# Performance work log

Measured on AMD Instinct MI355X. Metric: run time of the kernel, lower is better.

Reference implementation:

```python
import jax, jax.numpy as jnp
import numpy as np

CLS_W, REG_W, OBJ_W = 1.0, 5.0, 1.0
NUM_CLASSES = 30
B, N = 16, 64
SCALES = [(80, 80), (40, 40), (20, 20)]


def setup_inputs() -> dict:
    key = jax.random.key(0)
    ks = jax.random.split(key, 12)
    inp = {}
    for i, (h, w) in enumerate(SCALES):
        inp[f"cls_p{i}"] = jax.random.normal(ks[3 * i + 0], (B, NUM_CLASSES, h, w), jnp.float32)
        inp[f"reg_p{i}"] = jax.random.normal(ks[3 * i + 1], (B, 4, h, w), jnp.float32)
        inp[f"obj_p{i}"] = jax.random.normal(ks[3 * i + 2], (B, 1, h, w), jnp.float32)
    inp["boxes"] = jax.random.uniform(ks[9], (B, N, 4), jnp.float32)  # normalized cxcywh in [0,1)
    inp["labels"] = jax.random.randint(ks[10], (B, N), 0, NUM_CLASSES, jnp.int32)
    return inp


def _scale_losses(cls_p, reg_p, obj_p, boxes, labels):
    Bs, C, H, W = cls_p.shape
    # BCHW -> flat (B*H*W, C) to mirror the permute(0,2,3,1)
    cls_f = jnp.transpose(cls_p, (0, 2, 3, 1)).reshape(-1, C)
    reg_f = jnp.transpose(reg_p, (0, 2, 3, 1)).reshape(-1, 4)
    obj_f = jnp.transpose(obj_p, (0, 2, 3, 1)).reshape(-1)
    # grid assignment: int() truncation == floor for non-negative coords, then clamp
    gx = jnp.clip((boxes[..., 0] * W).astype(jnp.int32), 0, W - 1)
    gy = jnp.clip((boxes[..., 1] * H).astype(jnp.int32), 0, H - 1)
    bidx = jnp.arange(Bs, dtype=jnp.int32)[:, None]
    flat = ((bidx * H + gy) * W + gx).reshape(-1)  # [B*N] flat cell ids
    M = Bs * H * W
    obj_t = jnp.zeros((M,), cls_p.dtype).at[flat].set(1.0)
    reg_t = jnp.zeros((M, 4), cls_p.dtype).at[flat].set(boxes.reshape(-1, 4))
    cls_t = jnp.zeros((M, C), cls_p.dtype).at[flat, labels.reshape(-1)].set(1.0)
    pos = obj_t > 0.5
    npos = jnp.maximum(pos.sum().astype(cls_p.dtype), 1.0)
    # cross-entropy on positive cells (argmax of one-hot target, ties -> lowest idx as in torch)
    cls_idx = jnp.argmax(cls_t, axis=-1)
    ce = jax.nn.logsumexp(cls_f, axis=-1) - jnp.take_along_axis(cls_f, cls_idx[:, None], axis=-1)[:, 0]
    cls_loss = jnp.sum(jnp.where(pos, ce, 0.0)) / npos * CLS_W
    # smooth-L1 (beta=1), mean over 4 coords, clamp at 10, mean over positives
    d = jnp.abs(reg_f - reg_t)
    sl1 = jnp.mean(jnp.where(d < 1.0, 0.5 * d * d, d - 0.5), axis=-1)
    sl1 = jnp.minimum(sl1, 10.0)
    reg_loss = jnp.sum(jnp.where(pos, sl1, 0.0)) / npos * REG_W
    # BCE-with-logits over ALL cells: softplus(x) - x*t
    obj_loss = jnp.mean(jax.nn.softplus(obj_f) - obj_f * obj_t) * OBJ_W
    return cls_loss, reg_loss, obj_loss


def reference(cls_p0, cls_p1, cls_p2, reg_p0, reg_p1, reg_p2,
              obj_p0, obj_p1, obj_p2, boxes, labels):
    cls_list = [cls_p0, cls_p1, cls_p2]
    reg_list = [reg_p0, reg_p1, reg_p2]
    obj_list = [obj_p0, obj_p1, obj_p2]
    num_scales = len(cls_list)
    cls_sum = reg_sum = obj_sum = jnp.float32(0.0)
    for cp, rp, op in zip(cls_list, reg_list, obj_list):
        cl, rl, ol = _scale_losses(cp, rp, op, boxes, labels)
        cls_sum = cls_sum + cl
        reg_sum = reg_sum + rl
        obj_sum = obj_sum + ol
    cls_sum = cls_sum / num_scales
    reg_sum = reg_sum / num_scales
    obj_sum = obj_sum / num_scales
    total = cls_sum + reg_sum + obj_sum
    # stacked [total, cls, reg, obj] (dict in original)
    return jnp.stack([total, cls_sum, reg_sum, obj_sum])
```

## Files before the change

kernel.cpp:

```cpp
#include <hip/hip_runtime.h>
#include <math.h>

#define NCLS 30
#define OBJ_BLOCKS 132
#define POS_BLOCKS 12
#define NTASK 48


__device__ __forceinline__ float softplusf(float x) {
    return (x > 20.0f) ? x : log1pf(__expf(x));
}

__global__ __launch_bounds__(256) void detloss_main(
    const float* __restrict__ cls0, const float* __restrict__ reg0, const float* __restrict__ obj0,
    const float* __restrict__ cls1, const float* __restrict__ reg1, const float* __restrict__ obj1,
    const float* __restrict__ cls2, const float* __restrict__ reg2, const float* __restrict__ obj2,
    const float* __restrict__ boxes, const int* __restrict__ labels,
    float* __restrict__ ws)
{
    const int bx = blockIdx.x;
    const int tid = threadIdx.x;
    const int wave = tid >> 6;
    const int lane = tid & 63;

    if (bx < OBJ_BLOCKS) {
        float a0 = 0.0f, a1 = 0.0f, a2 = 0.0f;
        const int gi = bx * 256 + tid;
        if (gi < 33600) {
            const float4* p; int li;
            if (gi < 25600)      { p = (const float4*)obj0; li = gi; }
            else if (gi < 32000) { p = (const float4*)obj1; li = gi - 25600; }
            else                 { p = (const float4*)obj2; li = gi - 32000; }
            const float4 v = p[li];
            const float s = softplusf(v.x) + softplusf(v.y) + softplusf(v.z) + softplusf(v.w);
            if (gi < 25600) a0 = s; else if (gi < 32000) a1 = s; else a2 = s;
        }
        #pragma unroll
        for (int m = 32; m > 0; m >>= 1) {
            a0 += __shfl_xor(a0, m);
            a1 += __shfl_xor(a1, m);
            a2 += __shfl_xor(a2, m);
        }
        __shared__ float red[4][3];
        if (lane == 0) { red[wave][0] = a0; red[wave][1] = a1; red[wave][2] = a2; }
        __syncthreads();
        if (tid < 3) {
            ws[bx * 4 + tid] = red[0][tid] + red[1][tid] + red[2][tid] + red[3][tid];
        }
    } else {
        const int task  = (bx - OBJ_BLOCKS) * 4 + wave;
        const int scale = task >> 4;
        const int batch = task & 15;
        const float* cls; const float* reg; const float* obj; int H, W;
        if (scale == 0)      { cls = cls0; reg = reg0; obj = obj0; H = 80; W = 80; }
        else if (scale == 1) { cls = cls1; reg = reg1; obj = obj1; H = 40; W = 40; }
        else                 { cls = cls2; reg = reg2; obj = obj2; H = 20; W = 20; }
        const int HW = H * W;

        const int j = batch * 64 + lane;
        const float4 bv = ((const float4*)boxes)[j];
        const int lab = labels[j];
        int gx = (int)(bv.x * (float)W); gx = max(0, min(W - 1, gx));
        int gy = (int)(bv.y * (float)H); gy = max(0, min(H - 1, gy));
        const int cell = gy * W + gx;

        bool winner = true;
        int minlab = 1 << 30;
        for (int m = 0; m < 64; ++m) {
            const int oc = __shfl(cell, m);
            const int ol = __shfl(lab, m);
            if (oc == cell) {
                if (m > lane) winner = false;
                minlab = min(minlab, ol);
            }
        }

        float ce = 0.0f, sl = 0.0f, npos = 0.0f, po = 0.0f;
        if (winner) {
            const float* cb = cls + (size_t)batch * NCLS * HW + cell;
            float v[NCLS];
            float mx = -INFINITY;
            #pragma unroll
            for (int c = 0; c < NCLS; ++c) { v[c] = cb[(size_t)c * HW]; mx = fmaxf(mx, v[c]); }
            float se = 0.0f, tgt = 0.0f;
            #pragma unroll
            for (int c = 0; c < NCLS; ++c) {
                se += __expf(v[c] - mx);
                if (c == minlab) tgt = v[c];
            }
            ce = mx + __logf(se) - tgt;

            const float* rb = reg + (size_t)batch * 4 * HW + cell;
            const float t[4] = { bv.x, bv.y, bv.z, bv.w };
            #pragma unroll
            for (int k = 0; k < 4; ++k) {
                const float d = fabsf(rb[(size_t)k * HW] - t[k]);
                sl += (d < 1.0f) ? 0.5f * d * d : (d - 0.5f);
            }
            sl = fminf(sl * 0.25f, 10.0f);

            po = obj[(size_t)batch * HW + cell];
            npos = 1.0f;
        }
        #pragma unroll
        for (int m = 32; m > 0; m >>= 1) {
            ce   += __shfl_xor(ce, m);
            sl   += __shfl_xor(sl, m);
            npos += __shfl_xor(npos, m);
            po   += __shfl_xor(po, m);
        }
        if (lane == 0) {
            float* o = ws + (size_t)(OBJ_BLOCKS + task) * 4;
            o[0] = ce; o[1] = sl; o[2] = npos; o[3] = po;
        }
    }
}

__global__ __launch_bounds__(256) void detloss_final(
    const float* __restrict__ ws, float* __restrict__ out)
{
    const int tid = threadIdx.x;
    const int wave = tid >> 6;
    const int lane = tid & 63;

    float acc[15];
    #pragma unroll
    for (int k = 0; k < 15; ++k) acc[k] = 0.0f;

    for (int i = tid; i < OBJ_BLOCKS; i += 256) {
        acc[0] += ws[i * 4 + 0];
        acc[1] += ws[i * 4 + 1];
        acc[2] += ws[i * 4 + 2];
    }
    for (int t = tid; t < NTASK; t += 256) {
        const int s = t >> 4;
        const float* o = ws + (size_t)(OBJ_BLOCKS + t) * 4;
        acc[3 + s * 4 + 0] += o[0];
        acc[3 + s * 4 + 1] += o[1];
        acc[3 + s * 4 + 2] += o[2];
        acc[3 + s * 4 + 3] += o[3];
    }
    #pragma unroll
    for (int m = 32; m > 0; m >>= 1)
        #pragma unroll
        for (int k = 0; k < 15; ++k) acc[k] += __shfl_xor(acc[k], m);

    __shared__ float red[4][15];
    if (lane == 0)
        #pragma unroll
        for (int k = 0; k < 15; ++k) red[wave][k] = acc[k];
    __syncthreads();

    if (tid == 0) {
        float f[15];
        #pragma unroll
        for (int k = 0; k < 15; ++k) f[k] = red[0][k] + red[1][k] + red[2][k] + red[3][k];
        const float Ms[3] = { 16.0f * 6400.0f, 16.0f * 1600.0f, 16.0f * 400.0f };
        float clsl = 0.0f, regl = 0.0f, objl = 0.0f;
        for (int s = 0; s < 3; ++s) {
            const float npos = fmaxf(f[3 + s * 4 + 2], 1.0f);
            clsl += f[3 + s * 4 + 0] / npos;
            regl += 5.0f * f[3 + s * 4 + 1] / npos;
            objl += (f[s] - f[3 + s * 4 + 3]) / Ms[s];
        }
        clsl /= 3.0f; regl /= 3.0f; objl /= 3.0f;
        out[0] = clsl + regl + objl;
        out[1] = clsl;
        out[2] = regl;
        out[3] = objl;
    }
}

extern "C" void kernel_launch(void* const* d_in, const int* in_sizes, int n_in,
                              void* d_out, int out_size, void* d_ws, size_t ws_size,
                              hipStream_t stream) {
    const float* cls0   = (const float*)d_in[0];
    const float* reg0   = (const float*)d_in[1];
    const float* obj0   = (const float*)d_in[2];
    const float* cls1   = (const float*)d_in[3];
    const float* reg1   = (const float*)d_in[4];
    const float* obj1   = (const float*)d_in[5];
    const float* cls2   = (const float*)d_in[6];
    const float* reg2   = (const float*)d_in[7];
    const float* obj2   = (const float*)d_in[8];
    const float* boxes  = (const float*)d_in[9];
    const int*   labels = (const int*)d_in[10];
    float* ws  = (float*)d_ws;
    float* out = (float*)d_out;

    detloss_main<<<dim3(OBJ_BLOCKS + POS_BLOCKS), 256, 0, stream>>>(
        cls0, reg0, obj0, cls1, reg1, obj1, cls2, reg2, obj2,
        boxes, labels, ws);
    detloss_final<<<1, 256, 0, stream>>>(ws, out);
}
```

Measured before the change: 99.10 us.

## Fuse final reduction into main kernel via atomics and last-block counter

Replaces the separate single-block finalize kernel with global atomicAdd accumulation into 15 workspace slots, plus a completion counter. The last block to finish computes the final losses. A hipMemsetAsync zeroes the accumulators before the launch. This removes one kernel launch and its dependency gap, but adds a memset and atomic contention on a few addresses, and float atomics make the summation order non-deterministic.

```diff
diff --git a/kernel.cpp b/kernel.cpp
--- a/kernel.cpp
+++ b/kernel.cpp
@@ -4,19 +4,19 @@
 #define NCLS 30
 #define OBJ_BLOCKS 132
 #define POS_BLOCKS 12
-#define NTASK 48
+#define TOTAL_BLOCKS (OBJ_BLOCKS + POS_BLOCKS)
 
 
 __device__ __forceinline__ float softplusf(float x) {
     return (x > 20.0f) ? x : log1pf(__expf(x));
 }
 
-__global__ __launch_bounds__(256) void detloss_main(
+__global__ __launch_bounds__(256) void detloss_fused(
     const float* __restrict__ cls0, const float* __restrict__ reg0, const float* __restrict__ obj0,
     const float* __restrict__ cls1, const float* __restrict__ reg1, const float* __restrict__ obj1,
     const float* __restrict__ cls2, const float* __restrict__ reg2, const float* __restrict__ obj2,
     const float* __restrict__ boxes, const int* __restrict__ labels,
-    float* __restrict__ ws)
+    float* __restrict__ ws, float* __restrict__ out)
 {
     const int bx = blockIdx.x;
     const int tid = threadIdx.x;
@@ -45,7 +45,8 @@
         if (lane == 0) { red[wave][0] = a0; red[wave][1] = a1; red[wave][2] = a2; }
         __syncthreads();
         if (tid < 3) {
-            ws[bx * 4 + tid] = red[0][tid] + red[1][tid] + red[2][tid] + red[3][tid];
+            const float v = red[0][tid] + red[1][tid] + red[2][tid] + red[3][tid];
+            atomicAdd(&ws[tid * 5 + 0], v);
         }
     } else {
         const int task  = (bx - OBJ_BLOCKS) * 4 + wave;
@@ -110,64 +111,40 @@
             po   += __shfl_xor(po, m);
         }
         if (lane == 0) {
-            float* o = ws + (size_t)(OBJ_BLOCKS + task) * 4;
-            o[0] = ce; o[1] = sl; o[2] = npos; o[3] = po;
+            atomicAdd(&ws[scale * 5 + 1], ce);
+            atomicAdd(&ws[scale * 5 + 2], sl);
+            atomicAdd(&ws[scale * 5 + 3], npos);
+            atomicAdd(&ws[scale * 5 + 4], po);
         }
+        __syncthreads();
     }
-}
 
-__global__ __launch_bounds__(256) void detloss_final(
-    const float* __restrict__ ws, float* __restrict__ out)
-{
-    const int tid = threadIdx.x;
-    const int wave = tid >> 6;
-    const int lane = tid & 63;
-
-    float acc[15];
-    #pragma unroll
-    for (int k = 0; k < 15; ++k) acc[k] = 0.0f;
-
-    for (int i = tid; i < OBJ_BLOCKS; i += 256) {
-        acc[0] += ws[i * 4 + 0];
-        acc[1] += ws[i * 4 + 1];
-        acc[2] += ws[i * 4 + 2];
-    }
-    for (int t = tid; t < NTASK; t += 256) {
-        const int s = t >> 4;
-        const float* o = ws + (size_t)(OBJ_BLOCKS + t) * 4;
-        acc[3 + s * 4 + 0] += o[0];
-        acc[3 + s * 4 + 1] += o[1];
-        acc[3 + s * 4 + 2] += o[2];
-        acc[3 + s * 4 + 3] += o[3];
-    }
-    #pragma unroll
-    for (int m = 32; m > 0; m >>= 1)
-        #pragma unroll
-        for (int k = 0; k < 15; ++k) acc[k] += __shfl_xor(acc[k], m);
-
-    __shared__ float red[4][15];
-    if (lane == 0)
-        #pragma unroll
-        for (int k = 0; k < 15; ++k) red[wave][k] = acc[k];
-    __syncthreads();
-
+    if (bx < OBJ_BLOCKS) __syncthreads();
     if (tid == 0) {
-        float f[15];
-        #pragma unroll
-        for (int k = 0; k < 15; ++k) f[k] = red[0][k] + red[1][k] + red[2][k] + red[3][k];
-        const float Ms[3] = { 16.0f * 6400.0f, 16.0f * 1600.0f, 16.0f * 400.0f };
-        float clsl = 0.0f, regl = 0.0f, objl = 0.0f;
-        for (int s = 0; s < 3; ++s) {
-            const float npos = fmaxf(f[3 + s * 4 + 2], 1.0f);
-            clsl += f[3 + s * 4 + 0] / npos;
-            regl += 5.0f * f[3 + s * 4 + 1] / npos;
-            objl += (f[s] - f[3 + s * 4 + 3]) / Ms[s];
+        __threadfence();
+        unsigned* ctr = (unsigned*)ws + 15;
+        const unsigned old = atomicAdd(ctr, 1u);
+        if (old == TOTAL_BLOCKS - 1) {
+            __threadfence();
+            float f[15];
+            #pragma unroll
+            for (int k = 0; k < 15; ++k)
+                f[k] = __hip_atomic_load(&ws[k], __ATOMIC_RELAXED, __HIP_MEMORY_SCOPE_AGENT);
+            const float Ms[3] = { 16.0f * 6400.0f, 16.0f * 1600.0f, 16.0f * 400.0f };
+            float clsl = 0.0f, regl = 0.0f, objl = 0.0f;
+            #pragma unroll
+            for (int s = 0; s < 3; ++s) {
+                const float npos = fmaxf(f[s * 5 + 3], 1.0f);
+                clsl += f[s * 5 + 1] / npos;
+                regl += 5.0f * f[s * 5 + 2] / npos;
+                objl += (f[s * 5 + 0] - f[s * 5 + 4]) / Ms[s];
+            }
+            clsl /= 3.0f; regl /= 3.0f; objl /= 3.0f;
+            out[0] = clsl + regl + objl;
+            out[1] = clsl;
+            out[2] = regl;
+            out[3] = objl;
         }
-        clsl /= 3.0f; regl /= 3.0f; objl /= 3.0f;
-        out[0] = clsl + regl + objl;
-        out[1] = clsl;
-        out[2] = regl;
-        out[3] = objl;
     }
 }
 
@@ -188,8 +165,9 @@
     float* ws  = (float*)d_ws;
     float* out = (float*)d_out;
 
-    detloss_main<<<dim3(OBJ_BLOCKS + POS_BLOCKS), 256, 0, stream>>>(
+    hipMemsetAsync(ws, 0, 64, stream);
+
+    detloss_fused<<<dim3(TOTAL_BLOCKS), 256, 0, stream>>>(
         cls0, reg0, obj0, cls1, reg1, obj1, cls2, reg2, obj2,
-        boxes, labels, ws);
-    detloss_final<<<1, 256, 0, stream>>>(ws, out);
+        boxes, labels, ws, out);
 }
```

Measured after the change: 97.22 us (median of 2 runs). Within noise of the previous version (-1.9%).
